# Kernel tuning notes

Hardware: AMD Instinct MI355X
Metric: run time of the kernel (lower is better)

## Reference

```python
import jax, jax.numpy as jnp
import numpy as np

N_NODES = 100000
N_EDGES = 3200000
IN_FEAT = 128


def gcn_conv(x, src, dst, W, b, num_nodes):
    # PyG GCNConv: h = x @ W, then symmetric-normalized aggregation with self-loops.
    h = x @ W  # [N, out]
    # add self loops
    loop = jnp.arange(num_nodes, dtype=src.dtype)
    s = jnp.concatenate([src, loop])
    d = jnp.concatenate([dst, loop])
    # degree over destination (col) with unit edge weights
    deg = jax.ops.segment_sum(jnp.ones_like(s, dtype=h.dtype), d, num_segments=num_nodes)
    dinv = jnp.where(deg > 0, jax.lax.rsqrt(deg), 0.0)
    norm = dinv[s] * dinv[d]  # [E+N]
    msg = norm[:, None] * h[s]  # gather source features, scale per edge
    out = jax.ops.segment_sum(msg, d, num_segments=num_nodes)
    return out + b


def setup_inputs() -> dict:
    key = jax.random.key(0)
    ks = jax.random.split(key, 8)
    x = jax.random.normal(ks[0], (N_NODES, IN_FEAT), dtype=jnp.float32)
    edge_index = jax.random.randint(ks[1], (2, N_EDGES), 0, N_NODES, dtype=jnp.int64)
    def glorot(k, shape):
        lim = np.sqrt(6.0 / (shape[0] + shape[1]))
        return jax.random.uniform(k, shape, jnp.float32, -lim, lim)
    return {
        "x": x,
        "edge_index": edge_index,
        "W1": glorot(ks[2], (IN_FEAT, 4)), "b1": jnp.zeros((4,), jnp.float32),
        "W2": glorot(ks[3], (4, 2)),       "b2": jnp.zeros((2,), jnp.float32),
        "W3": glorot(ks[4], (2, 1)),       "b3": jnp.zeros((1,), jnp.float32),
    }


def reference(x, edge_index, W1, b1, W2, b2, W3, b3):
    src, dst = edge_index[0], edge_index[1]
    n = x.shape[0]
    h = gcn_conv(x, src, dst, W1, b1, n)
    h = jax.nn.relu(h)
    # F.dropout(training=self.training): inference mode -> identity
    h = gcn_conv(h, src, dst, W2, b2, n)
    h = jax.nn.relu(h)
    h = gcn_conv(h, src, dst, W3, b3, n)
    return jax.nn.sigmoid(h)  # [N, 1]
```

## Files before the change

### kernel.cpp

```cpp
#include <hip/hip_runtime.h>
#include <hip/hip_bf16.h>
#include <math.h>


#define TPB 256
#define CHUNK 4096
#define EPT (CHUNK / TPB)
#define SLAB2 9216
#define NSMAX 1024

__global__ __launch_bounds__(TPB) void k_part(
    const int* __restrict__ src, const int* __restrict__ dst,
    unsigned int* __restrict__ slab, int* __restrict__ lstart,
    int NB, int NBP, int E)
{
    __shared__ int hist[512];
    __shared__ int s[TPB];
    __shared__ unsigned int sorted[CHUNK];
    int t = threadIdx.x;
    int base = blockIdx.x * CHUNK;
    int n = min(CHUNK, E - base);
    hist[t] = 0; hist[t + 256] = 0;
    __syncthreads();
    unsigned int meta[EPT];
#pragma unroll
    for (int k = 0; k < EPT; ++k) {
        int li = k * TPB + t;
        if (li < n) {
            int d = dst[base + li];
            int lp = atomicAdd(&hist[d >> 8], 1);
            meta[k] = ((unsigned)d << 13) | (unsigned)lp;
        } else meta[k] = 0xFFFFFFFFu;
    }
    __syncthreads();
    int run = 0;
    for (int cb = 0; cb < 512; cb += TPB) {
        int v = hist[cb + t];
        s[t] = v;
        __syncthreads();
        int x = v;
        for (int d = 1; d < TPB; d <<= 1) {
            int y = (t >= d) ? s[t - d] : 0;
            __syncthreads();
            x += y; s[t] = x;
            __syncthreads();
        }
        hist[cb + t] = run + (x - v);
        run += s[TPB - 1];
        __syncthreads();
    }
#pragma unroll
    for (int k = 0; k < EPT; ++k) {
        if (meta[k] != 0xFFFFFFFFu) {
            unsigned m = meta[k];
            int d = (int)(m >> 13);
            int lp = (int)(m & 0x1FFFu);
            unsigned p = (unsigned)src[base + k * TPB + t] | ((unsigned)(d & 255) << 17);
            sorted[hist[d >> 8] + lp] = p;
        }
    }
    __syncthreads();
    const uint4* s4 = (const uint4*)sorted;
    uint4* g4 = (uint4*)(slab + (size_t)base);
    for (int i = t; i < CHUNK / 4; i += TPB) g4[i] = s4[i];
    for (int i = t; i < NBP; i += TPB)
        lstart[(size_t)blockIdx.x * NBP + i] = (i < NB) ? hist[i] : n;
}

__global__ __launch_bounds__(TPB) void k_degree(
    const unsigned int* __restrict__ slab, const int* __restrict__ lstart,
    int* __restrict__ ssrc, int* __restrict__ cnt, int* __restrict__ off,
    float* __restrict__ dinv, int NS, int NBP, int N)
{
    __shared__ unsigned int pl[SLAB2];
    __shared__ int slen[NSMAX];
    __shared__ int s[TPB];
    __shared__ int c[TPB];
    __shared__ int cur[TPB];
    int t = threadIdx.x, b = blockIdx.x;
    c[t] = 0;
    int stv[NSMAX / TPB], lenv[NSMAX / TPB];
#pragma unroll
    for (int ci = 0; ci < NSMAX / TPB; ++ci) {
        int j = ci * TPB + t;
        int st = 0, len = 0;
        if (j < NS) {
            st = lstart[(size_t)j * NBP + b];
            len = lstart[(size_t)j * NBP + b + 1] - st;
        }
        stv[ci] = st; lenv[ci] = len;
        slen[j] = len;
    }
    __syncthreads();
    int run = 0;
    for (int cb = 0; cb < NSMAX; cb += TPB) {
        int v = slen[cb + t];
        s[t] = v;
        __syncthreads();
        int x = v;
        for (int d = 1; d < TPB; d <<= 1) {
            int y = (t >= d) ? s[t - d] : 0;
            __syncthreads();
            x += y; s[t] = x;
            __syncthreads();
        }
        slen[cb + t] = run + (x - v);
        run += s[TPB - 1];
        __syncthreads();
    }
    int total = min(run, SLAB2);
#pragma unroll
    for (int ci = 0; ci < NSMAX / TPB; ++ci) {
        int j = ci * TPB + t;
        if (j < NS && lenv[ci] > 0) {
            int lo = slen[j];
            const unsigned int* sp = slab + (size_t)j * CHUNK + stv[ci];
            for (int k = 0; k < lenv[ci]; ++k) {
                if (lo + k >= SLAB2) break;
                pl[lo + k] = sp[k];
            }
        }
    }
    __syncthreads();
    for (int i = t; i < total; i += TPB) atomicAdd(&c[(pl[i] >> 17) & 255], 1);
    __syncthreads();
    int cv = c[t];
    s[t] = cv;
    __syncthreads();
    int x = cv;
    for (int d = 1; d < TPB; d <<= 1) {
        int y = (t >= d) ? s[t - d] : 0;
        __syncthreads();
        x += y; s[t] = x;
        __syncthreads();
    }
    int excl = x - cv;
    int v = (b << 8) + t;
    if (v < N) {
        cnt[v] = cv;
        off[v] = b * SLAB2 + excl;
        dinv[v] = rsqrtf((float)(cv + 1));
    }
    cur[t] = excl;
    __syncthreads();
    int* sb = ssrc + (size_t)b * SLAB2;
    for (int i = t; i < total; i += TPB) {
        unsigned p = pl[i];
        int pos = atomicAdd(&cur[(p >> 17) & 255], 1);
        sb[pos] = (int)(p & 0x1FFFFu);
    }
}

__global__ __launch_bounds__(TPB) void k_node1(
    const float* __restrict__ x, const float* __restrict__ W1,
    const float* __restrict__ dinv, float* __restrict__ hs1, int n) {
    __shared__ float Ws[512];
    for (int i = threadIdx.x; i < 512; i += TPB) Ws[i] = W1[i];
    __syncthreads();
    int t = blockIdx.x * TPB + threadIdx.x;
    int v = t >> 2, p = t & 3;
    if (v >= n) return;
    const float4* xr = (const float4*)(x + (size_t)v * 128);
    float a0 = 0.f, a1 = 0.f, a2 = 0.f, a3 = 0.f;
#pragma unroll
    for (int i = 0; i < 8; ++i) {
        int c = p + i * 4;
        float4 xx = xr[c];
        const float* w = &Ws[c * 16];
        a0 += xx.x * w[0] + xx.y * w[4] + xx.z * w[8]  + xx.w * w[12];
        a1 += xx.x * w[1] + xx.y * w[5] + xx.z * w[9]  + xx.w * w[13];
        a2 += xx.x * w[2] + xx.y * w[6] + xx.z * w[10] + xx.w * w[14];
        a3 += xx.x * w[3] + xx.y * w[7] + xx.z * w[11] + xx.w * w[15];
    }
    a0 += __shfl_xor(a0, 1); a0 += __shfl_xor(a0, 2);
    a1 += __shfl_xor(a1, 1); a1 += __shfl_xor(a1, 2);
    a2 += __shfl_xor(a2, 1); a2 += __shfl_xor(a2, 2);
    a3 += __shfl_xor(a3, 1); a3 += __shfl_xor(a3, 2);
    if (p == 0) {
        float di = dinv[v];
        ((float4*)hs1)[v] = make_float4(di * a0, di * a1, di * a2, di * a3);
    }
}

__global__ __launch_bounds__(TPB) void k_gather1(
    const int* __restrict__ off, const int* __restrict__ cnt,
    const int* __restrict__ ssrc, const float* __restrict__ hs1,
    const float* __restrict__ dinv, const float* __restrict__ b1,
    const float* __restrict__ W2, float* __restrict__ hs2, int n) {
    int t = blockIdx.x * TPB + threadIdx.x;
    int v = t >> 3, p = t & 7;
    if (v >= n) return;
    int base = off[v], c = cnt[v];
    float4 acc = make_float4(0.f, 0.f, 0.f, 0.f);
    for (int i = p; i < c; i += 8) {
        int s = ssrc[base + i];
        float4 h = ((const float4*)hs1)[s];
        acc.x += h.x; acc.y += h.y; acc.z += h.z; acc.w += h.w;
    }
    acc.x += __shfl_xor(acc.x, 1); acc.x += __shfl_xor(acc.x, 2); acc.x += __shfl_xor(acc.x, 4);
    acc.y += __shfl_xor(acc.y, 1); acc.y += __shfl_xor(acc.y, 2); acc.y += __shfl_xor(acc.y, 4);
    acc.z += __shfl_xor(acc.z, 1); acc.z += __shfl_xor(acc.z, 2); acc.z += __shfl_xor(acc.z, 4);
    acc.w += __shfl_xor(acc.w, 1); acc.w += __shfl_xor(acc.w, 2); acc.w += __shfl_xor(acc.w, 4);
    if (p == 0) {
        float4 hv = ((const float4*)hs1)[v];
        float di = dinv[v];
        float o0 = fmaxf(di * (acc.x + hv.x) + b1[0], 0.f);
        float o1 = fmaxf(di * (acc.y + hv.y) + b1[1], 0.f);
        float o2 = fmaxf(di * (acc.z + hv.z) + b1[2], 0.f);
        float o3 = fmaxf(di * (acc.w + hv.w) + b1[3], 0.f);
        float h0 = o0 * W2[0] + o1 * W2[2] + o2 * W2[4] + o3 * W2[6];
        float h1 = o0 * W2[1] + o1 * W2[3] + o2 * W2[5] + o3 * W2[7];
        ((float2*)hs2)[v] = make_float2(di * h0, di * h1);
    }
}

__global__ __launch_bounds__(TPB) void k_gather2(
    const int* __restrict__ off, const int* __restrict__ cnt,
    const int* __restrict__ ssrc, const float* __restrict__ hs2,
    const float* __restrict__ dinv, const float* __restrict__ b2,
    const float* __restrict__ W3, float* __restrict__ hs3, int n) {
    int t = blockIdx.x * TPB + threadIdx.x;
    int v = t >> 3, p = t & 7;
    if (v >= n) return;
    int base = off[v], c = cnt[v];
    float2 acc = make_float2(0.f, 0.f);
    for (int i = p; i < c; i += 8) {
        int s = ssrc[base + i];
        float2 h = ((const float2*)hs2)[s];
        acc.x += h.x; acc.y += h.y;
    }
    acc.x += __shfl_xor(acc.x, 1); acc.x += __shfl_xor(acc.x, 2); acc.x += __shfl_xor(acc.x, 4);
    acc.y += __shfl_xor(acc.y, 1); acc.y += __shfl_xor(acc.y, 2); acc.y += __shfl_xor(acc.y, 4);
    if (p == 0) {
        float2 hv = ((const float2*)hs2)[v];
        float di = dinv[v];
        float o0 = fmaxf(di * (acc.x + hv.x) + b2[0], 0.f);
        float o1 = fmaxf(di * (acc.y + hv.y) + b2[1], 0.f);
        float h3 = o0 * W3[0] + o1 * W3[1];
        hs3[v] = di * h3;
    }
}

__global__ __launch_bounds__(TPB) void k_gather3(
    const int* __restrict__ off, const int* __restrict__ cnt,
    const int* __restrict__ ssrc, const float* __restrict__ hs3,
    const float* __restrict__ dinv, const float* __restrict__ b3,
    float* __restrict__ out, int n) {
    int t = blockIdx.x * TPB + threadIdx.x;
    int v = t >> 3, p = t & 7;
    if (v >= n) return;
    int base = off[v], c = cnt[v];
    float acc = 0.f;
    for (int i = p; i < c; i += 8) acc += hs3[ssrc[base + i]];
    acc += __shfl_xor(acc, 1); acc += __shfl_xor(acc, 2); acc += __shfl_xor(acc, 4);
    if (p == 0) {
        float di = dinv[v];
        float agg = di * (acc + hs3[v]) + b3[0];
        out[v] = 1.0f / (1.0f + __expf(-agg));
    }
}

extern "C" void kernel_launch(void* const* d_in, const int* in_sizes, int n_in,
                              void* d_out, int out_size, void* d_ws, size_t ws_size,
                              hipStream_t stream) {
    const float* x  = (const float*)d_in[0];
    const int* ei   = (const int*)d_in[1];
    const float* W1 = (const float*)d_in[2];
    const float* b1 = (const float*)d_in[3];
    const float* W2 = (const float*)d_in[4];
    const float* b2 = (const float*)d_in[5];
    const float* W3 = (const float*)d_in[6];
    const float* b3 = (const float*)d_in[7];
    float* out = (float*)d_out;

    const int N = in_sizes[0] / 128;
    const int E = in_sizes[1] / 2;
    const int* src = ei;
    const int* dst = ei + E;

    const int NS  = (E + CHUNK - 1) / CHUNK;
    const int NB  = (N + 255) >> 8;
    const int NBP = NB + 1;

    char* w = (char*)d_ws;
    auto carve = [&](size_t bytes) { char* p = w; w += (bytes + 15) & ~(size_t)15; return p; };
    unsigned int* slab = (unsigned int*)carve((size_t)NS * CHUNK * 4);
    int* lstart        = (int*)carve((size_t)NS * NBP * 4);
    int* ssrc          = (int*)carve((size_t)NB * SLAB2 * 4);
    int* cnt           = (int*)carve((size_t)N * 4);
    int* off           = (int*)carve((size_t)N * 4);
    float* dinv        = (float*)carve((size_t)N * 4);
    float* hs1 = (float*)slab;
    float* hs2 = hs1 + (size_t)4 * N;
    float* hs3 = hs2 + (size_t)2 * N;

    const int nbN4 = (4 * N + TPB - 1) / TPB;
    const int nbN8 = (8 * N + TPB - 1) / TPB;

    k_part   <<<NS, TPB, 0, stream>>>(src, dst, slab, lstart, NB, NBP, E);
    k_degree <<<NB, TPB, 0, stream>>>(slab, lstart, ssrc, cnt, off, dinv, NS, NBP, N);
    k_node1  <<<nbN4, TPB, 0, stream>>>(x, W1, dinv, hs1, N);
    k_gather1<<<nbN8, TPB, 0, stream>>>(off, cnt, ssrc, hs1, dinv, b1, W2, hs2, N);
    k_gather2<<<nbN8, TPB, 0, stream>>>(off, cnt, ssrc, hs2, dinv, b2, W3, hs3, N);
    k_gather3<<<nbN8, TPB, 0, stream>>>(off, cnt, ssrc, hs3, dinv, b3, out, N);
}
```

Measured before the change: 216.6 us.

## Fuse x@W1 into degree kernel, use wave-shuffle scans and transposed segment starts

Extra blocks are appended to the degree kernel to compute the unnormalized x@W1 projection alongside the CSR build, so the dense projection no longer waits for degrees. The dinv[src] scaling moves into the first gather, which adds one extra gathered load per edge. Block scans now use 64-lane shuffle scans in place of the multi-barrier shared-memory scans. The lstart table is written transposed so the degree kernel reads it coalesced, the slab copy is spread over 8 lanes per segment, and off/cnt are packed into a single int2.

```diff
diff --git a/kernel.cpp b/kernel.cpp
--- a/kernel.cpp
+++ b/kernel.cpp
@@ -1,5 +1,4 @@
 #include <hip/hip_runtime.h>
-#include <hip/hip_bf16.h>
 #include <math.h>
 
 
@@ -11,11 +10,11 @@
 
 __global__ __launch_bounds__(TPB) void k_part(
     const int* __restrict__ src, const int* __restrict__ dst,
-    unsigned int* __restrict__ slab, int* __restrict__ lstart,
-    int NB, int NBP, int E)
+    unsigned int* __restrict__ slab, int* __restrict__ lstartT,
+    int NB, int NBP, int NS, int E)
 {
     __shared__ int hist[512];
-    __shared__ int s[TPB];
+    __shared__ int wtot[4];
     __shared__ unsigned int sorted[CHUNK];
     int t = threadIdx.x;
     int base = blockIdx.x * CHUNK;
@@ -33,30 +32,32 @@
         } else meta[k] = 0xFFFFFFFFu;
     }
     __syncthreads();
-    int run = 0;
-    for (int cb = 0; cb < 512; cb += TPB) {
-        int v = hist[cb + t];
-        s[t] = v;
-        __syncthreads();
-        int x = v;
-        for (int d = 1; d < TPB; d <<= 1) {
-            int y = (t >= d) ? s[t - d] : 0;
-            __syncthreads();
-            x += y; s[t] = x;
-            __syncthreads();
-        }
-        hist[cb + t] = run + (x - v);
-        run += s[TPB - 1];
-        __syncthreads();
-    }
+    int v0 = hist[2 * t], v1 = hist[2 * t + 1];
+    int pr = v0 + v1;
+    int x = pr;
+    int lane = t & 63;
+    for (int d = 1; d < 64; d <<= 1) {
+        int y = __shfl_up(x, d);
+        if (lane >= d) x += y;
+    }
+    if (lane == 63) wtot[t >> 6] = x;
+    __syncthreads();
+    int w = t >> 6;
+    int woff = 0;
+#pragma unroll
+    for (int i = 0; i < 4; ++i) if (i < w) woff += wtot[i];
+    int excl = woff + x - pr;
+    hist[2 * t] = excl;
+    hist[2 * t + 1] = excl + v0;
+    __syncthreads();
 #pragma unroll
     for (int k = 0; k < EPT; ++k) {
         if (meta[k] != 0xFFFFFFFFu) {
             unsigned m = meta[k];
             int d = (int)(m >> 13);
             int lp = (int)(m & 0x1FFFu);
-            unsigned p = (unsigned)src[base + k * TPB + t] | ((unsigned)(d & 255) << 17);
-            sorted[hist[d >> 8] + lp] = p;
+            unsigned pk = (unsigned)src[base + k * TPB + t] | ((unsigned)(d & 255) << 17);
+            sorted[hist[d >> 8] + lp] = pk;
         }
     }
     __syncthreads();
@@ -64,165 +65,175 @@
     uint4* g4 = (uint4*)(slab + (size_t)base);
     for (int i = t; i < CHUNK / 4; i += TPB) g4[i] = s4[i];
     for (int i = t; i < NBP; i += TPB)
-        lstart[(size_t)blockIdx.x * NBP + i] = (i < NB) ? hist[i] : n;
+        lstartT[(size_t)i * NS + blockIdx.x] = (i < NB) ? hist[i] : n;
 }
 
 __global__ __launch_bounds__(TPB) void k_degree(
-    const unsigned int* __restrict__ slab, const int* __restrict__ lstart,
-    int* __restrict__ ssrc, int* __restrict__ cnt, int* __restrict__ off,
-    float* __restrict__ dinv, int NS, int NBP, int N)
+    const unsigned int* __restrict__ slab, const int* __restrict__ lstartT,
+    int* __restrict__ ssrc, int2* __restrict__ oc, float* __restrict__ dinv,
+    const float* __restrict__ x, const float* __restrict__ W1,
+    float* __restrict__ h1, int NS, int NB, int N)
 {
     __shared__ unsigned int pl[SLAB2];
+    __shared__ int sstart[NSMAX];
     __shared__ int slen[NSMAX];
-    __shared__ int s[TPB];
     __shared__ int c[TPB];
     __shared__ int cur[TPB];
-    int t = threadIdx.x, b = blockIdx.x;
+    __shared__ int wtot[4];
+    int t = threadIdx.x;
+
+    if (blockIdx.x >= NB) {
+        float* Ws = (float*)pl;
+        for (int i = t; i < 512; i += TPB) Ws[i] = W1[i];
+        __syncthreads();
+        int tt = (blockIdx.x - NB) * TPB + t;
+        int v = tt >> 2, p = tt & 3;
+        if (v >= N) return;
+        const float4* xr = (const float4*)(x + (size_t)v * 128);
+        float a0 = 0.f, a1 = 0.f, a2 = 0.f, a3 = 0.f;
+#pragma unroll
+        for (int i = 0; i < 8; ++i) {
+            int cc = p + i * 4;
+            float4 xx = xr[cc];
+            const float* wv = &Ws[cc * 16];
+            a0 += xx.x * wv[0] + xx.y * wv[4] + xx.z * wv[8]  + xx.w * wv[12];
+            a1 += xx.x * wv[1] + xx.y * wv[5] + xx.z * wv[9]  + xx.w * wv[13];
+            a2 += xx.x * wv[2] + xx.y * wv[6] + xx.z * wv[10] + xx.w * wv[14];
+            a3 += xx.x * wv[3] + xx.y * wv[7] + xx.z * wv[11] + xx.w * wv[15];
+        }
+        a0 += __shfl_xor(a0, 1); a0 += __shfl_xor(a0, 2);
+        a1 += __shfl_xor(a1, 1); a1 += __shfl_xor(a1, 2);
+        a2 += __shfl_xor(a2, 1); a2 += __shfl_xor(a2, 2);
+        a3 += __shfl_xor(a3, 1); a3 += __shfl_xor(a3, 2);
+        if (p == 0) ((float4*)h1)[v] = make_float4(a0, a1, a2, a3);
+        return;
+    }
+
+    int b = blockIdx.x;
     c[t] = 0;
-    int stv[NSMAX / TPB], lenv[NSMAX / TPB];
-#pragma unroll
-    for (int ci = 0; ci < NSMAX / TPB; ++ci) {
-        int j = ci * TPB + t;
+    for (int j = t; j < NSMAX; j += TPB) {
         int st = 0, len = 0;
         if (j < NS) {
-            st = lstart[(size_t)j * NBP + b];
-            len = lstart[(size_t)j * NBP + b + 1] - st;
+            st = lstartT[(size_t)b * NS + j];
+            len = lstartT[(size_t)(b + 1) * NS + j] - st;
         }
-        stv[ci] = st; lenv[ci] = len;
+        sstart[j] = st;
         slen[j] = len;
     }
     __syncthreads();
-    int run = 0;
-    for (int cb = 0; cb < NSMAX; cb += TPB) {
-        int v = slen[cb + t];
-        s[t] = v;
-        __syncthreads();
-        int x = v;
-        for (int d = 1; d < TPB; d <<= 1) {
-            int y = (t >= d) ? s[t - d] : 0;
-            __syncthreads();
-            x += y; s[t] = x;
-            __syncthreads();
+    int s0 = slen[4 * t], s1 = slen[4 * t + 1], s2 = slen[4 * t + 2], s3 = slen[4 * t + 3];
+    int pq = s0 + s1 + s2 + s3;
+    int xs = pq;
+    int lane = t & 63;
+    for (int d = 1; d < 64; d <<= 1) {
+        int y = __shfl_up(xs, d);
+        if (lane >= d) xs += y;
+    }
+    if (lane == 63) wtot[t >> 6] = xs;
+    __syncthreads();
+    int w = t >> 6;
+    int woff = 0, tot = 0;
+#pragma unroll
+    for (int i = 0; i < 4; ++i) { int z = wtot[i]; tot += z; if (i < w) woff += z; }
+    int e0 = woff + xs - pq;
+    slen[4 * t]     = e0;
+    slen[4 * t + 1] = e0 + s0;
+    slen[4 * t + 2] = e0 + s0 + s1;
+    slen[4 * t + 3] = e0 + s0 + s1 + s2;
+    __syncthreads();
+    int total = min(tot, SLAB2);
+    int g = t >> 3, l = t & 7;
+    for (int j0 = 0; j0 < NS; j0 += 32) {
+        int j = j0 + g;
+        if (j < NS) {
+            int lo = slen[j];
+            int len = slen[j + 1] - lo;
+            int lim = min(len, SLAB2 - lo);
+            const unsigned int* sp = slab + (size_t)j * CHUNK + sstart[j];
+            for (int k = l; k < lim; k += 8) pl[lo + k] = sp[k];
         }
-        slen[cb + t] = run + (x - v);
-        run += s[TPB - 1];
-        __syncthreads();
-    }
-    int total = min(run, SLAB2);
-#pragma unroll
-    for (int ci = 0; ci < NSMAX / TPB; ++ci) {
-        int j = ci * TPB + t;
-        if (j < NS && lenv[ci] > 0) {
-            int lo = slen[j];
-            const unsigned int* sp = slab + (size_t)j * CHUNK + stv[ci];
-            for (int k = 0; k < lenv[ci]; ++k) {
-                if (lo + k >= SLAB2) break;
-                pl[lo + k] = sp[k];
-            }
-        }
     }
     __syncthreads();
     for (int i = t; i < total; i += TPB) atomicAdd(&c[(pl[i] >> 17) & 255], 1);
     __syncthreads();
     int cv = c[t];
-    s[t] = cv;
-    __syncthreads();
-    int x = cv;
-    for (int d = 1; d < TPB; d <<= 1) {
-        int y = (t >= d) ? s[t - d] : 0;
-        __syncthreads();
-        x += y; s[t] = x;
-        __syncthreads();
-    }
-    int excl = x - cv;
+    int xc = cv;
+    for (int d = 1; d < 64; d <<= 1) {
+        int y = __shfl_up(xc, d);
+        if (lane >= d) xc += y;
+    }
+    if (lane == 63) wtot[t >> 6] = xc;
+    __syncthreads();
+    int woff2 = 0;
+#pragma unroll
+    for (int i = 0; i < 4; ++i) if (i < w) woff2 += wtot[i];
+    int excl = woff2 + xc - cv;
     int v = (b << 8) + t;
     if (v < N) {
-        cnt[v] = cv;
-        off[v] = b * SLAB2 + excl;
+        oc[v] = make_int2(b * SLAB2 + excl, cv);
         dinv[v] = rsqrtf((float)(cv + 1));
     }
     cur[t] = excl;
     __syncthreads();
     int* sb = ssrc + (size_t)b * SLAB2;
     for (int i = t; i < total; i += TPB) {
-        unsigned p = pl[i];
-        int pos = atomicAdd(&cur[(p >> 17) & 255], 1);
-        sb[pos] = (int)(p & 0x1FFFFu);
-    }
-}
-
-__global__ __launch_bounds__(TPB) void k_node1(
-    const float* __restrict__ x, const float* __restrict__ W1,
-    const float* __restrict__ dinv, float* __restrict__ hs1, int n) {
-    __shared__ float Ws[512];
-    for (int i = threadIdx.x; i < 512; i += TPB) Ws[i] = W1[i];
-    __syncthreads();
-    int t = blockIdx.x * TPB + threadIdx.x;
-    int v = t >> 2, p = t & 3;
-    if (v >= n) return;
-    const float4* xr = (const float4*)(x + (size_t)v * 128);
-    float a0 = 0.f, a1 = 0.f, a2 = 0.f, a3 = 0.f;
-#pragma unroll
-    for (int i = 0; i < 8; ++i) {
-        int c = p + i * 4;
-        float4 xx = xr[c];
-        const float* w = &Ws[c * 16];
-        a0 += xx.x * w[0] + xx.y * w[4] + xx.z * w[8]  + xx.w * w[12];
-        a1 += xx.x * w[1] + xx.y * w[5] + xx.z * w[9]  + xx.w * w[13];
-        a2 += xx.x * w[2] + xx.y * w[6] + xx.z * w[10] + xx.w * w[14];
-        a3 += xx.x * w[3] + xx.y * w[7] + xx.z * w[11] + xx.w * w[15];
-    }
-    a0 += __shfl_xor(a0, 1); a0 += __shfl_xor(a0, 2);
-    a1 += __shfl_xor(a1, 1); a1 += __shfl_xor(a1, 2);
-    a2 += __shfl_xor(a2, 1); a2 += __shfl_xor(a2, 2);
-    a3 += __shfl_xor(a3, 1); a3 += __shfl_xor(a3, 2);
-    if (p == 0) {
-        float di = dinv[v];
-        ((float4*)hs1)[v] = make_float4(di * a0, di * a1, di * a2, di * a3);
+        unsigned pk = pl[i];
+        int pos = atomicAdd(&cur[(pk >> 17) & 255], 1);
+        sb[pos] = (int)(pk & 0x1FFFFu);
     }
 }
 
 __global__ __launch_bounds__(TPB) void k_gather1(
-    const int* __restrict__ off, const int* __restrict__ cnt,
-    const int* __restrict__ ssrc, const float* __restrict__ hs1,
-    const float* __restrict__ dinv, const float* __restrict__ b1,
-    const float* __restrict__ W2, float* __restrict__ hs2, int n) {
+    const int2* __restrict__ oc, const int* __restrict__ ssrc,
+    const float* __restrict__ h1, const float* __restrict__ dinv,
+    const float* __restrict__ b1, const float* __restrict__ W2,
+    float* __restrict__ hs2, int n) {
     int t = blockIdx.x * TPB + threadIdx.x;
     int v = t >> 3, p = t & 7;
     if (v >= n) return;
-    int base = off[v], c = cnt[v];
+    int2 ocv = oc[v];
+    int base = ocv.x, c = ocv.y;
     float4 acc = make_float4(0.f, 0.f, 0.f, 0.f);
     for (int i = p; i < c; i += 8) {
         int s = ssrc[base + i];
-        float4 h = ((const float4*)hs1)[s];
-        acc.x += h.x; acc.y += h.y; acc.z += h.z; acc.w += h.w;
+        float ds = dinv[s];
+        float4 h = ((const float4*)h1)[s];
+        acc.x += __fmul_rn(ds, h.x);
+        acc.y += __fmul_rn(ds, h.y);
+        acc.z += __fmul_rn(ds, h.z);
+        acc.w += __fmul_rn(ds, h.w);
     }
     acc.x += __shfl_xor(acc.x, 1); acc.x += __shfl_xor(acc.x, 2); acc.x += __shfl_xor(acc.x, 4);
     acc.y += __shfl_xor(acc.y, 1); acc.y += __shfl_xor(acc.y, 2); acc.y += __shfl_xor(acc.y, 4);
     acc.z += __shfl_xor(acc.z, 1); acc.z += __shfl_xor(acc.z, 2); acc.z += __shfl_xor(acc.z, 4);
     acc.w += __shfl_xor(acc.w, 1); acc.w += __shfl_xor(acc.w, 2); acc.w += __shfl_xor(acc.w, 4);
     if (p == 0) {
-        float4 hv = ((const float4*)hs1)[v];
         float di = dinv[v];
-        float o0 = fmaxf(di * (acc.x + hv.x) + b1[0], 0.f);
-        float o1 = fmaxf(di * (acc.y + hv.y) + b1[1], 0.f);
-        float o2 = fmaxf(di * (acc.z + hv.z) + b1[2], 0.f);
-        float o3 = fmaxf(di * (acc.w + hv.w) + b1[3], 0.f);
-        float h0 = o0 * W2[0] + o1 * W2[2] + o2 * W2[4] + o3 * W2[6];
-        float h1 = o0 * W2[1] + o1 * W2[3] + o2 * W2[5] + o3 * W2[7];
-        ((float2*)hs2)[v] = make_float2(di * h0, di * h1);
+        float4 hv = ((const float4*)h1)[v];
+        float h0 = __fmul_rn(di, hv.x);
+        float h1v = __fmul_rn(di, hv.y);
+        float h2 = __fmul_rn(di, hv.z);
+        float h3 = __fmul_rn(di, hv.w);
+        float o0 = fmaxf(di * (acc.x + h0)  + b1[0], 0.f);
+        float o1 = fmaxf(di * (acc.y + h1v) + b1[1], 0.f);
+        float o2 = fmaxf(di * (acc.z + h2)  + b1[2], 0.f);
+        float o3 = fmaxf(di * (acc.w + h3)  + b1[3], 0.f);
+        float g0 = o0 * W2[0] + o1 * W2[2] + o2 * W2[4] + o3 * W2[6];
+        float g1 = o0 * W2[1] + o1 * W2[3] + o2 * W2[5] + o3 * W2[7];
+        ((float2*)hs2)[v] = make_float2(di * g0, di * g1);
     }
 }
 
 __global__ __launch_bounds__(TPB) void k_gather2(
-    const int* __restrict__ off, const int* __restrict__ cnt,
-    const int* __restrict__ ssrc, const float* __restrict__ hs2,
-    const float* __restrict__ dinv, const float* __restrict__ b2,
-    const float* __restrict__ W3, float* __restrict__ hs3, int n) {
+    const int2* __restrict__ oc, const int* __restrict__ ssrc,
+    const float* __restrict__ hs2, const float* __restrict__ dinv,
+    const float* __restrict__ b2, const float* __restrict__ W3,
+    float* __restrict__ hs3, int n) {
     int t = blockIdx.x * TPB + threadIdx.x;
     int v = t >> 3, p = t & 7;
     if (v >= n) return;
-    int base = off[v], c = cnt[v];
+    int2 ocv = oc[v];
+    int base = ocv.x, c = ocv.y;
     float2 acc = make_float2(0.f, 0.f);
     for (int i = p; i < c; i += 8) {
         int s = ssrc[base + i];
@@ -242,14 +253,14 @@
 }
 
 __global__ __launch_bounds__(TPB) void k_gather3(
-    const int* __restrict__ off, const int* __restrict__ cnt,
-    const int* __restrict__ ssrc, const float* __restrict__ hs3,
-    const float* __restrict__ dinv, const float* __restrict__ b3,
-    float* __restrict__ out, int n) {
+    const int2* __restrict__ oc, const int* __restrict__ ssrc,
+    const float* __restrict__ hs3, const float* __restrict__ dinv,
+    const float* __restrict__ b3, float* __restrict__ out, int n) {
     int t = blockIdx.x * TPB + threadIdx.x;
     int v = t >> 3, p = t & 7;
     if (v >= n) return;
-    int base = off[v], c = cnt[v];
+    int2 ocv = oc[v];
+    int base = ocv.x, c = ocv.y;
     float acc = 0.f;
     for (int i = p; i < c; i += 8) acc += hs3[ssrc[base + i]];
     acc += __shfl_xor(acc, 1); acc += __shfl_xor(acc, 2); acc += __shfl_xor(acc, 4);
@@ -285,22 +296,20 @@
     char* w = (char*)d_ws;
     auto carve = [&](size_t bytes) { char* p = w; w += (bytes + 15) & ~(size_t)15; return p; };
     unsigned int* slab = (unsigned int*)carve((size_t)NS * CHUNK * 4);
-    int* lstart        = (int*)carve((size_t)NS * NBP * 4);
+    int* lstartT       = (int*)carve((size_t)NBP * NS * 4);
     int* ssrc          = (int*)carve((size_t)NB * SLAB2 * 4);
-    int* cnt           = (int*)carve((size_t)N * 4);
-    int* off           = (int*)carve((size_t)N * 4);
+    int2* oc           = (int2*)carve((size_t)N * 8);
     float* dinv        = (float*)carve((size_t)N * 4);
-    float* hs1 = (float*)slab;
-    float* hs2 = hs1 + (size_t)4 * N;
+    float* h1          = (float*)carve((size_t)4 * N * 4);
+    float* hs2 = (float*)slab;
     float* hs3 = hs2 + (size_t)2 * N;
 
-    const int nbN4 = (4 * N + TPB - 1) / TPB;
+    const int nb1  = (4 * N + TPB - 1) / TPB;
     const int nbN8 = (8 * N + TPB - 1) / TPB;
 
-    k_part   <<<NS, TPB, 0, stream>>>(src, dst, slab, lstart, NB, NBP, E);
-    k_degree <<<NB, TPB, 0, stream>>>(slab, lstart, ssrc, cnt, off, dinv, NS, NBP, N);
-    k_node1  <<<nbN4, TPB, 0, stream>>>(x, W1, dinv, hs1, N);
-    k_gather1<<<nbN8, TPB, 0, stream>>>(off, cnt, ssrc, hs1, dinv, b1, W2, hs2, N);
-    k_gather2<<<nbN8, TPB, 0, stream>>>(off, cnt, ssrc, hs2, dinv, b2, W3, hs3, N);
-    k_gather3<<<nbN8, TPB, 0, stream>>>(off, cnt, ssrc, hs3, dinv, b3, out, N);
-}
+    k_part   <<<NS, TPB, 0, stream>>>(src, dst, slab, lstartT, NB, NBP, NS, E);
+    k_degree <<<NB + nb1, TPB, 0, stream>>>(slab, lstartT, ssrc, oc, dinv, x, W1, h1, NS, NB, N);
+    k_gather1<<<nbN8, TPB, 0, stream>>>(oc, ssrc, h1, dinv, b1, W2, hs2, N);
+    k_gather2<<<nbN8, TPB, 0, stream>>>(oc, ssrc, hs2, dinv, b2, W3, hs3, N);
+    k_gather3<<<nbN8, TPB, 0, stream>>>(oc, ssrc, hs3, dinv, b3, out, N);
+}
```

After: 222.2 us. 1.03x slower.

## Use wavefront shuffle scans and transpose bucket-start table for coalesced reads

Applied to the files above, without the earlier changes.

Replaces the shared-memory Hillis-Steele prefix scans in the partition and degree kernels with 64-lane shuffle scans plus a small per-wave total combine, which removes many block-wide barriers. It also stores the per-chunk bucket start offsets transposed, so the degree kernel reads each bucket's starts contiguously across chunks instead of with a large stride. In exchange, the partition kernel now writes those offsets with a strided pattern. The total length is taken from the last exclusive-scan slot, which relies on the padded entries having zero length.

```diff
diff --git a/kernel.cpp b/kernel.cpp
--- a/kernel.cpp
+++ b/kernel.cpp
@@ -1,5 +1,4 @@
 #include <hip/hip_runtime.h>
-#include <hip/hip_bf16.h>
 #include <math.h>
 
 
@@ -11,12 +10,12 @@
 
 __global__ __launch_bounds__(TPB) void k_part(
     const int* __restrict__ src, const int* __restrict__ dst,
-    unsigned int* __restrict__ slab, int* __restrict__ lstart,
-    int NB, int NBP, int E)
+    unsigned int* __restrict__ slab, int* __restrict__ lstartT,
+    int NB, int NBP, int NS, int E)
 {
     __shared__ int hist[512];
-    __shared__ int s[TPB];
     __shared__ unsigned int sorted[CHUNK];
+    __shared__ int wtot[4];
     int t = threadIdx.x;
     int base = blockIdx.x * CHUNK;
     int n = min(CHUNK, E - base);
@@ -33,22 +32,24 @@
         } else meta[k] = 0xFFFFFFFFu;
     }
     __syncthreads();
-    int run = 0;
-    for (int cb = 0; cb < 512; cb += TPB) {
-        int v = hist[cb + t];
-        s[t] = v;
-        __syncthreads();
-        int x = v;
-        for (int d = 1; d < TPB; d <<= 1) {
-            int y = (t >= d) ? s[t - d] : 0;
-            __syncthreads();
-            x += y; s[t] = x;
-            __syncthreads();
-        }
-        hist[cb + t] = run + (x - v);
-        run += s[TPB - 1];
-        __syncthreads();
-    }
+    int v0 = hist[2 * t], v1 = hist[2 * t + 1];
+    int pr = v0 + v1;
+    int x = pr;
+    int lane = t & 63;
+    for (int d = 1; d < 64; d <<= 1) {
+        int y = __shfl_up(x, d);
+        if (lane >= d) x += y;
+    }
+    if (lane == 63) wtot[t >> 6] = x;
+    __syncthreads();
+    int w = t >> 6;
+    int woff = 0;
+#pragma unroll
+    for (int i = 0; i < 4; ++i) if (i < w) woff += wtot[i];
+    int excl = woff + x - pr;
+    hist[2 * t] = excl;
+    hist[2 * t + 1] = excl + v0;
+    __syncthreads();
 #pragma unroll
     for (int k = 0; k < EPT; ++k) {
         if (meta[k] != 0xFFFFFFFFu) {
@@ -64,19 +65,19 @@
     uint4* g4 = (uint4*)(slab + (size_t)base);
     for (int i = t; i < CHUNK / 4; i += TPB) g4[i] = s4[i];
     for (int i = t; i < NBP; i += TPB)
-        lstart[(size_t)blockIdx.x * NBP + i] = (i < NB) ? hist[i] : n;
+        lstartT[(size_t)i * NS + blockIdx.x] = (i < NB) ? hist[i] : n;
 }
 
 __global__ __launch_bounds__(TPB) void k_degree(
-    const unsigned int* __restrict__ slab, const int* __restrict__ lstart,
+    const unsigned int* __restrict__ slab, const int* __restrict__ lstartT,
     int* __restrict__ ssrc, int* __restrict__ cnt, int* __restrict__ off,
-    float* __restrict__ dinv, int NS, int NBP, int N)
+    float* __restrict__ dinv, int NS, int NB, int N)
 {
     __shared__ unsigned int pl[SLAB2];
     __shared__ int slen[NSMAX];
-    __shared__ int s[TPB];
     __shared__ int c[TPB];
     __shared__ int cur[TPB];
+    __shared__ int wtot[4];
     int t = threadIdx.x, b = blockIdx.x;
     c[t] = 0;
     int stv[NSMAX / TPB], lenv[NSMAX / TPB];
@@ -85,30 +86,28 @@
         int j = ci * TPB + t;
         int st = 0, len = 0;
         if (j < NS) {
-            st = lstart[(size_t)j * NBP + b];
-            len = lstart[(size_t)j * NBP + b + 1] - st;
+            st  = lstartT[(size_t)b * NS + j];
+            len = lstartT[(size_t)(b + 1) * NS + j] - st;
         }
         stv[ci] = st; lenv[ci] = len;
         slen[j] = len;
     }
     __syncthreads();
-    int run = 0;
-    for (int cb = 0; cb < NSMAX; cb += TPB) {
-        int v = slen[cb + t];
-        s[t] = v;
-        __syncthreads();
-        int x = v;
-        for (int d = 1; d < TPB; d <<= 1) {
-            int y = (t >= d) ? s[t - d] : 0;
-            __syncthreads();
-            x += y; s[t] = x;
-            __syncthreads();
-        }
-        slen[cb + t] = run + (x - v);
-        run += s[TPB - 1];
-        __syncthreads();
-    }
-    int total = min(run, SLAB2);
+    int lane = t & 63, w = t >> 6;
+    int s0 = slen[4*t], s1 = slen[4*t+1], s2 = slen[4*t+2], s3 = slen[4*t+3];
+    int pq = s0 + s1 + s2 + s3, xs = pq;
+    for (int d = 1; d < 64; d <<= 1) { int y = __shfl_up(xs, d); if (lane >= d) xs += y; }
+    if (lane == 63) wtot[w] = xs;
+    __syncthreads();
+    int woff = 0;
+#pragma unroll
+    for (int i = 0; i < 4; ++i) if (i < w) woff += wtot[i];
+    int e0 = woff + xs - pq;
+    slen[4*t]   = e0;
+    slen[4*t+1] = e0 + s0;
+    slen[4*t+2] = e0 + s0 + s1;
+    slen[4*t+3] = e0 + s0 + s1 + s2;
+    __syncthreads();
 #pragma unroll
     for (int ci = 0; ci < NSMAX / TPB; ++ci) {
         int j = ci * TPB + t;
@@ -122,19 +121,21 @@
         }
     }
     __syncthreads();
+    int total = 0;
+    {
+        total = min(slen[NSMAX - 1], SLAB2);
+    }
     for (int i = t; i < total; i += TPB) atomicAdd(&c[(pl[i] >> 17) & 255], 1);
     __syncthreads();
     int cv = c[t];
-    s[t] = cv;
-    __syncthreads();
-    int x = cv;
-    for (int d = 1; d < TPB; d <<= 1) {
-        int y = (t >= d) ? s[t - d] : 0;
-        __syncthreads();
-        x += y; s[t] = x;
-        __syncthreads();
-    }
-    int excl = x - cv;
+    int xc = cv;
+    for (int d = 1; d < 64; d <<= 1) { int y = __shfl_up(xc, d); if (lane >= d) xc += y; }
+    if (lane == 63) wtot[w] = xc;
+    __syncthreads();
+    int woff2 = 0;
+#pragma unroll
+    for (int i = 0; i < 4; ++i) if (i < w) woff2 += wtot[i];
+    int excl = woff2 + xc - cv;
     int v = (b << 8) + t;
     if (v < N) {
         cnt[v] = cv;
@@ -285,7 +286,7 @@
     char* w = (char*)d_ws;
     auto carve = [&](size_t bytes) { char* p = w; w += (bytes + 15) & ~(size_t)15; return p; };
     unsigned int* slab = (unsigned int*)carve((size_t)NS * CHUNK * 4);
-    int* lstart        = (int*)carve((size_t)NS * NBP * 4);
+    int* lstartT       = (int*)carve((size_t)NBP * NS * 4);
     int* ssrc          = (int*)carve((size_t)NB * SLAB2 * 4);
     int* cnt           = (int*)carve((size_t)N * 4);
     int* off           = (int*)carve((size_t)N * 4);
@@ -297,8 +298,8 @@
     const int nbN4 = (4 * N + TPB - 1) / TPB;
     const int nbN8 = (8 * N + TPB - 1) / TPB;
 
-    k_part   <<<NS, TPB, 0, stream>>>(src, dst, slab, lstart, NB, NBP, E);
-    k_degree <<<NB, TPB, 0, stream>>>(slab, lstart, ssrc, cnt, off, dinv, NS, NBP, N);
+    k_part   <<<NS, TPB, 0, stream>>>(src, dst, slab, lstartT, NB, NBP, NS, E);
+    k_degree <<<NB, TPB, 0, stream>>>(slab, lstartT, ssrc, cnt, off, dinv, NS, NB, N);
     k_node1  <<<nbN4, TPB, 0, stream>>>(x, W1, dinv, hs1, N);
     k_gather1<<<nbN8, TPB, 0, stream>>>(off, cnt, ssrc, hs1, dinv, b1, W2, hs2, N);
     k_gather2<<<nbN8, TPB, 0, stream>>>(off, cnt, ssrc, hs2, dinv, b2, W3, hs3, N);
```

Result: no change. 214.9 us (-0.8%).
